# Kernel tuning notes

Hardware: AMD Instinct MI355X
Metric: run time of the kernel (lower is better)

Reference implementation:

```python
import jax, jax.numpy as jnp
import numpy as np
from jax import lax

DIM = 96
KS = 7
EPS = 1e-6


def setup_inputs() -> dict:
    key = jax.random.key(0)
    ks = jax.random.split(key, 12)
    N, C, H, W = 64, DIM, 56, 56
    s = 0.02
    x = jax.random.normal(ks[0], (N, C, H, W), dtype=jnp.float32)
    dw_w = jax.random.normal(ks[1], (C, 1, KS, KS), dtype=jnp.float32) * s  # depthwise, OIHW with I=1
    dw_b = jnp.zeros((C,), dtype=jnp.float32)
    ln_g = jnp.ones((C,), dtype=jnp.float32)
    ln_b = jnp.zeros((C,), dtype=jnp.float32)
    w1 = jax.random.normal(ks[2], (4 * C, C), dtype=jnp.float32) * s   # torch Linear weight [out,in]
    b1 = jnp.zeros((4 * C,), dtype=jnp.float32)
    grn_g = jnp.zeros((4 * C,), dtype=jnp.float32)  # GRN gamma/beta init to 0 as in ConvNeXtV2
    grn_b = jnp.zeros((4 * C,), dtype=jnp.float32)
    w2 = jax.random.normal(ks[3], (C, 4 * C), dtype=jnp.float32) * s
    b2 = jnp.zeros((C,), dtype=jnp.float32)
    return {"x": x, "dw_w": dw_w, "dw_b": dw_b, "ln_g": ln_g, "ln_b": ln_b,
            "w1": w1, "b1": b1, "grn_g": grn_g, "grn_b": grn_b, "w2": w2, "b2": b2}


def reference(x, dw_w, dw_b, ln_g, ln_b, w1, b1, grn_g, grn_b, w2, b2):
    C = x.shape[1]
    pad = KS // 2
    # 7x7 depthwise conv, NCHW
    y = lax.conv_general_dilated(x, dw_w, window_strides=(1, 1),
                                 padding=[(pad, pad), (pad, pad)],
                                 dimension_numbers=("NCHW", "OIHW", "NCHW"),
                                 feature_group_count=C)
    y = y + dw_b[None, :, None, None]
    y = jnp.transpose(y, (0, 2, 3, 1))  # [N,H,W,C]
    # channels-last LayerNorm, eps=1e-6
    mu = jnp.mean(y, axis=-1, keepdims=True)
    var = jnp.mean(jnp.square(y - mu), axis=-1, keepdims=True)
    y = (y - mu) * lax.rsqrt(var + EPS) * ln_g + ln_b
    # pwconv1 -> GELU (exact erf, torch default)
    y = jnp.einsum("nhwc,fc->nhwf", y, w1) + b1
    y = jax.nn.gelu(y, approximate=False)
    # GRN over spatial dims
    gx = jnp.sqrt(jnp.sum(jnp.square(y), axis=(1, 2), keepdims=True))  # [N,1,1,4C]
    nx = gx / (jnp.mean(gx, axis=-1, keepdims=True) + EPS)
    y = grn_g * (y * nx) + grn_b + y
    # pwconv2
    y = jnp.einsum("nhwf,cf->nhwc", y, w2) + b2
    y = jnp.transpose(y, (0, 3, 1, 2))  # back to NCHW
    # drop_path=0.0 -> identity; residual add
    return x + y
```

## Files before the change

kernel.cpp:

```cpp
#include <hip/hip_runtime.h>
#include <hip/hip_bf16.h>
#include <math.h>

#define HW   3136
#define NIMG 64
#define M_TOT (NIMG * HW)

typedef __attribute__((ext_vector_type(8))) short bf16x8_t;
typedef __attribute__((ext_vector_type(4))) float f32x4_t;
typedef __bf16 bf16x2v __attribute__((ext_vector_type(2)));

__device__ __forceinline__ unsigned short f2bf(float f) {
  union { float f; unsigned u; } v; v.f = f;
  unsigned r = v.u + 0x7FFFu + ((v.u >> 16) & 1u);
  return (unsigned short)(r >> 16);
}
__device__ __forceinline__ float bf2f(unsigned short h) {
  union { unsigned u; float f; } v; v.u = ((unsigned)h) << 16;
  return v.f;
}

__device__ __forceinline__ float dot2bf(unsigned a, unsigned b, float c) {
#if __has_builtin(__builtin_amdgcn_fdot2_f32_bf16)
  return __builtin_amdgcn_fdot2_f32_bf16(__builtin_bit_cast(bf16x2v, a),
                                         __builtin_bit_cast(bf16x2v, b), c, false);
#else
  return c + bf2f((unsigned short)(a & 0xffffu)) * bf2f((unsigned short)(b & 0xffffu))
           + bf2f((unsigned short)(a >> 16)) * bf2f((unsigned short)(b >> 16));
#endif
}

__device__ __forceinline__ int xcd_swz(int bid0) {
  return ((bid0 & 7) * 392) + (bid0 >> 3);
}

__global__ void k0_swz(const float* __restrict__ wsrc, unsigned short* __restrict__ bsw,
                       int N, int K) {
  int idx = blockIdx.x * 256 + threadIdx.x;
  int total = (N / 16) * (K / 32) * 64;
  if (idx >= total) return;
  int l  = idx & 63;
  int fi = idx >> 6;
  int KT = K / 32;
  int nt = fi / KT, kt = fi - nt * KT;
  int nn = nt * 16 + (l & 15);
  int kb = kt * 32 + (l >> 4) * 8;
  const float* src = wsrc + (size_t)nn * K + kb;
  unsigned short* dst = bsw + (size_t)idx * 8;
#pragma unroll
  for (int j = 0; j < 8; j++) dst[j] = f2bf(src[j]);
}

__global__ void k0_b2p(const float* __restrict__ w2, const float* __restrict__ grnb,
                       const float* __restrict__ b2, float* __restrict__ b2p) {
  int c = blockIdx.x * blockDim.x + threadIdx.x;
  if (c >= 96) return;
  float s = b2[c];
  const float* wr = w2 + (size_t)c * 384;
  for (int f = 0; f < 384; f++) s += grnb[f] * wr[f];
  b2p[c] = s;
}

__global__ void k0w(const float* __restrict__ dww, unsigned short* __restrict__ wswz) {
  int i = blockIdx.x * 256 + threadIdx.x;
  if (i >= 96 * 56) return;
  int ch = i / 56, rem = i - ch * 56, dy = rem >> 3, dx = rem & 7;
  wswz[i] = (dx < 7) ? f2bf(dww[ch * 49 + dy * 7 + dx]) : (unsigned short)0;
}

__global__ __launch_bounds__(256, 3) void k12f(
    const float* __restrict__ x, const unsigned short* __restrict__ wswz,
    const float* __restrict__ dwb, const float* __restrict__ lng,
    const float* __restrict__ lnb, const unsigned short* __restrict__ B1,
    const float* __restrict__ b1, unsigned char* __restrict__ y1f8,
    float* __restrict__ gx2) {
  __shared__ char smem[28928];
  float* lnp = (float*)smem;
  unsigned short* xsh = (unsigned short*)(smem + 768);
  unsigned short (*ts)[104] = (unsigned short(*)[104])(smem + 15616);
  unsigned char* ytB = (unsigned char*)(smem + 768);

  const int t = threadIdx.x;
  const int bid = xcd_swz(blockIdx.x);
  const int n = bid / 49;
  const int tile = bid - n * 49;
  const int tr = tile / 7, tc = tile - tr * 7;
  const int h0 = tr * 8, w0 = tc * 8;

  if (t < 192) lnp[t] = (t < 96) ? lng[t] : lnb[t - 96];

  const int cch = t & 31, crow = t >> 5;
  const bool colInt = (tc >= 1) && (tc <= 5);
  const bool rowInt = (tr >= 1) && (tr <= 5);

  int g_r[7], g_ch[7], g_wb[7];
  bool g_hok[7];
#pragma unroll
  for (int k = 0; k < 7; k++) {
    int i = t + k * 256;
    int cq = i & 3;
    int rc = i >> 2;
    g_r[k] = rc % 14; g_ch[k] = rc / 14;
    g_wb[k] = w0 + cq * 4 - 3;
    g_hok[k] = (unsigned)(h0 + g_r[k] - 3) < 56u;
  }

  float4 raw[3][7];
#pragma unroll
  for (int cc = 0; cc < 3; cc++) {
#pragma unroll
    for (int k = 0; k < 7; k++) {
      const int h = h0 + g_r[k] - 3;
      const int wb = g_wb[k];
      const float* xb = x + (size_t)(n * 96 + cc * 32 + g_ch[k]) * HW + h * 56 + wb;
      float4 v;
      if (rowInt && colInt) {
        v = *(const float4*)xb;
      } else {
        v = make_float4(0.f, 0.f, 0.f, 0.f);
        if (g_hok[k]) {
          if (colInt) {
            v = *(const float4*)xb;
          } else {
            if ((unsigned)(wb + 0) < 56u) v.x = xb[0];
            if ((unsigned)(wb + 1) < 56u) v.y = xb[1];
            if ((unsigned)(wb + 2) < 56u) v.z = xb[2];
            if ((unsigned)(wb + 3) < 56u) v.w = xb[3];
          }
        }
      }
      raw[cc][k] = v;
    }
  }

#pragma unroll
  for (int cc = 0; cc < 3; cc++) {
    const int c0 = cc * 32;
    if (cc) __syncthreads();
#pragma unroll
    for (int k = 0; k < 7; k++) {
      float4 v = raw[cc][k];
      uint2 u;
      u.x = (unsigned)f2bf(v.x) | ((unsigned)f2bf(v.y) << 16);
      u.y = (unsigned)f2bf(v.z) | ((unsigned)f2bf(v.w) << 16);
      *(uint2*)&xsh[g_ch[k] * 232 + g_r[k] * 16 + (g_wb[k] - w0 + 3)] = u;
    }
    bf16x8_t wv[7];
#pragma unroll
    for (int dy = 0; dy < 7; dy++)
      wv[dy] = *(const bf16x8_t*)&wswz[(size_t)(c0 + cch) * 56 + dy * 8];
    const float bias = dwb[c0 + cch];
    __syncthreads();
    float acc[8];
#pragma unroll
    for (int j = 0; j < 8; j++) acc[j] = bias;
#pragma unroll
    for (int dy = 0; dy < 7; dy++) {
      const unsigned* pr = (const unsigned*)&xsh[cch * 232 + (crow + dy) * 16];
      uint4 pa = *(const uint4*)pr;
      uint4 pb = *(const uint4*)(pr + 4);
      unsigned p[8] = {pa.x, pa.y, pa.z, pa.w, pb.x, pb.y, pb.z, pb.w};
      unsigned q[7];
#pragma unroll
      for (int i = 0; i < 7; i++) q[i] = (p[i] >> 16) | (p[i + 1] << 16);
      const unsigned* wu = (const unsigned*)&wv[dy];
#pragma unroll
      for (int j = 0; j < 8; j += 2) {
        int b = j >> 1;
        acc[j] = dot2bf(wu[3], p[b + 3],
                 dot2bf(wu[2], p[b + 2],
                 dot2bf(wu[1], p[b + 1],
                 dot2bf(wu[0], p[b + 0], acc[j]))));
        acc[j + 1] = dot2bf(wu[3], q[b + 3],
                     dot2bf(wu[2], q[b + 2],
                     dot2bf(wu[1], q[b + 1],
                     dot2bf(wu[0], q[b + 0], acc[j + 1]))));
      }
    }
#pragma unroll
    for (int j = 0; j < 8; j++)
      ts[crow * 8 + j][c0 + cch] = f2bf(acc[j]);
  }
  __syncthreads();

  {
    const int px = t >> 2, q = t & 3;
    const unsigned onebf = 0x3F803F80u;
    unsigned vu[12];
    float s = 0.f, ss = 0.f;
#pragma unroll
    for (int j = 0; j < 12; j++) {
      vu[j] = *(const unsigned*)&ts[px][q * 24 + j * 2];
      s  = dot2bf(vu[j], onebf, s);
      ss = dot2bf(vu[j], vu[j], ss);
    }
    s  += __shfl_xor(s, 1);  s  += __shfl_xor(s, 2);
    ss += __shfl_xor(ss, 1); ss += __shfl_xor(ss, 2);
    float mu  = s * (1.f / 96.f);
    float var = ss * (1.f / 96.f) - mu * mu;
    float rs  = rsqrtf(var + 1e-6f);
#pragma unroll
    for (int j = 0; j < 12; j++) {
      int ch = q * 24 + j * 2;
      float v0 = bf2f((unsigned short)(vu[j] & 0xffffu));
      float v1 = bf2f((unsigned short)(vu[j] >> 16));
      float o0 = (v0 - mu) * rs * lnp[ch] + lnp[96 + ch];
      float o1 = (v1 - mu) * rs * lnp[ch + 1] + lnp[96 + ch + 1];
      *(unsigned*)&ts[px][ch] = (unsigned)f2bf(o0) | ((unsigned)f2bf(o1) << 16);
    }
  }
  __syncthreads();
  const int wv_ = t >> 6, l = t & 63;
  const int lg = l >> 4, lr = l & 15;
  bf16x8_t af[4][3];
#pragma unroll
  for (int mt = 0; mt < 4; mt++)
#pragma unroll
    for (int kt = 0; kt < 3; kt++)
      af[mt][kt] = *(const bf16x8_t*)&ts[mt * 16 + lr][kt * 32 + lg * 8];
  __syncthreads();

  for (int half = 0; half < 2; half++) {
    for (int i = 0; i < 3; i++) {
      const int ntl = wv_ * 3 + i;
      const int nt  = half * 12 + ntl;
      bf16x8_t bf[3];
#pragma unroll
      for (int kt = 0; kt < 3; kt++)
        bf[kt] = *(const bf16x8_t*)(B1 + ((size_t)(nt * 3 + kt) * 64 + l) * 8);
      f32x4_t acc[4];
#pragma unroll
      for (int mt = 0; mt < 4; mt++) {
        f32x4_t a = {0.f, 0.f, 0.f, 0.f};
#pragma unroll
        for (int kt = 0; kt < 3; kt++)
          a = __builtin_amdgcn_mfma_f32_16x16x32_bf16(af[mt][kt], bf[kt], a, 0, 0, 0);
        acc[mt] = a;
      }
      const int f0 = nt * 16, fl0 = ntl * 16;
      float bias = b1[f0 + lr];
      float s2 = 0.f;
#pragma unroll
      for (int mt = 0; mt < 4; mt++) {
#pragma unroll
        for (int r = 0; r < 4; r++) {
          float v = acc[mt][r] + bias;
          float sq = v * v;
          float pe = fmaf(sq, -0.10295294f, -2.3021183f);
          float e  = __builtin_amdgcn_exp2f(v * pe);
          float g  = v * __builtin_amdgcn_rcpf(1.f + e);
          s2 += g * g;
          unsigned p8 = (unsigned)__builtin_amdgcn_cvt_pk_fp8_f32(g, g, 0, false);
          ytB[(mt * 16 + lg * 4 + r) * 200 + fl0 + lr] = (unsigned char)p8;
        }
      }
      s2 += __shfl_xor(s2, 16);
      s2 += __shfl_xor(s2, 32);
      if (l < 16) atomicAdd(gx2 + n * 384 + f0 + l, s2);
    }
    __syncthreads();
#pragma unroll
    for (int it = 0; it < 6; it++) {
      int id = t + it * 256;
      int mt = id / 384, ktl = (id >> 6) % 6, ll = id & 63;
      unsigned long long d =
        *(const unsigned long long*)&ytB[(mt * 16 + (ll & 15)) * 200 + ktl * 32 + (ll >> 4) * 8];
      *(unsigned long long*)(y1f8 +
        (((size_t)(bid * 4 + mt) * 12 + half * 6 + ktl) * 64 + ll) * 8) = d;
    }
    __syncthreads();
  }
}

__global__ __launch_bounds__(256) void k3_coefB(
    const float* __restrict__ gx2, const float* __restrict__ grng,
    const unsigned short* __restrict__ B2, unsigned char* __restrict__ B2s8) {
  __shared__ float red[256];
  __shared__ float cf[384];
  const int n = blockIdx.x, t = threadIdx.x;
  float s = 0.f;
  for (int f = t; f < 384; f += 256) {
    float g = sqrtf(gx2[n * 384 + f]);
    cf[f] = g; s += g;
  }
  red[t] = s; __syncthreads();
  for (int o = 128; o > 0; o >>= 1) {
    if (t < o) red[t] += red[t + o];
    __syncthreads();
  }
  float inv = 1.f / (red[0] * (1.f / 384.f) + 1e-6f);
  for (int f = t; f < 384; f += 256)
    cf[f] = 1.f + grng[f] * cf[f] * inv;
  __syncthreads();
  unsigned char* dstn = B2s8 + (size_t)n * 36864;
  for (int i = t; i < 4608; i += 256) {
    int e0 = i * 8;
    int fi = e0 >> 9, ll = (e0 & 511) >> 3;
    int kb = (fi % 12) * 32 + (ll >> 4) * 8;
    uint4 w = *(const uint4*)(B2 + e0);
    const unsigned* wu = (const unsigned*)&w;
    float vv[8];
#pragma unroll
    for (int h = 0; h < 4; h++) {
      vv[h * 2 + 0] = bf2f((unsigned short)(wu[h] & 0xffffu)) * cf[kb + h * 2];
      vv[h * 2 + 1] = bf2f((unsigned short)(wu[h] >> 16)) * cf[kb + h * 2 + 1];
    }
    unsigned p0 = (unsigned)__builtin_amdgcn_cvt_pk_fp8_f32(vv[0], vv[1], 0, false);
    p0 = (unsigned)__builtin_amdgcn_cvt_pk_fp8_f32(vv[2], vv[3], p0, true);
    unsigned p1 = (unsigned)__builtin_amdgcn_cvt_pk_fp8_f32(vv[4], vv[5], 0, false);
    p1 = (unsigned)__builtin_amdgcn_cvt_pk_fp8_f32(vv[6], vv[7], p1, true);
    uint2 o; o.x = p0; o.y = p1;
    *(uint2*)(dstn + e0) = o;
  }
}

__global__ __launch_bounds__(256) void k4_gemm2(
    const unsigned char* __restrict__ y1f8, const unsigned char* __restrict__ B2s8,
    const float* __restrict__ b2p, const float* __restrict__ x,
    float* __restrict__ out) {
  __shared__ float zt[96][68];
  const int t  = threadIdx.x;
  const int wv = t >> 6, l = t & 63;
  const int lg = l >> 4, lr = l & 15;
  const int bid = xcd_swz(blockIdx.x);
  const int n = bid / 49;
  const int tile = bid - n * 49;
  const int tr = tile / 7, tc = tile - tr * 7;
  const unsigned char* Bn = B2s8 + (size_t)n * 36864;

  long af[12];
  const unsigned char* ap = y1f8 + ((size_t)(bid * 4 + wv) * 12) * 512 + l * 8;
#pragma unroll
  for (int kt = 0; kt < 12; kt++)
    af[kt] = *(const long*)(ap + kt * 512);

  f32x4_t acc[6];
#pragma unroll
  for (int i = 0; i < 6; i++) acc[i] = (f32x4_t){0.f, 0.f, 0.f, 0.f};
#pragma unroll
  for (int kt = 0; kt < 12; kt++) {
#pragma unroll
    for (int nt = 0; nt < 6; nt++) {
      long b = *(const long*)(Bn + ((size_t)(nt * 12 + kt) * 64 + l) * 8);
      acc[nt] = __builtin_amdgcn_mfma_f32_16x16x32_fp8_fp8(af[kt], b, acc[nt], 0, 0, 0);
    }
  }
#pragma unroll
  for (int nt = 0; nt < 6; nt++) {
    int c = nt * 16 + lr;
#pragma unroll
    for (int r = 0; r < 4; r++)
      zt[c][wv * 16 + lg * 4 + r] = acc[nt][r];
  }
  __syncthreads();
#pragma unroll
  for (int it = 0; it < 6; it++) {
    int id = t + it * 256;
    int c = id >> 4, q = id & 15;
    int row = q >> 1, jq = (q & 1) * 4;
    float4 z = *(const float4*)&zt[c][row * 8 + jq];
    size_t base = ((size_t)(n * 96 + c)) * HW + (size_t)(tr * 8 + row) * 56 + tc * 8 + jq;
    float4 xv = *(const float4*)(x + base);
    float bp = b2p[c];
    float4 o;
    o.x = xv.x + z.x + bp;
    o.y = xv.y + z.y + bp;
    o.z = xv.z + z.z + bp;
    o.w = xv.w + z.w + bp;
    *(float4*)(out + base) = o;
  }
}

extern "C" void kernel_launch(void* const* d_in, const int* in_sizes, int n_in,
                              void* d_out, int out_size, void* d_ws, size_t ws_size,
                              hipStream_t stream) {
  const float* x    = (const float*)d_in[0];
  const float* dww  = (const float*)d_in[1];
  const float* dwb  = (const float*)d_in[2];
  const float* lng  = (const float*)d_in[3];
  const float* lnb  = (const float*)d_in[4];
  const float* w1   = (const float*)d_in[5];
  const float* b1   = (const float*)d_in[6];
  const float* grng = (const float*)d_in[7];
  const float* grnb = (const float*)d_in[8];
  const float* w2   = (const float*)d_in[9];
  const float* b2   = (const float*)d_in[10];
  float* out = (float*)d_out;

  char* ws = (char*)d_ws;
  size_t off = 0;
  auto alloc = [&](size_t bytes) {
    char* p = ws + off;
    off += (bytes + 255) & ~(size_t)255;
    return p;
  };
  unsigned char*  y1f8 = (unsigned char*)alloc((size_t)M_TOT * 384);
  unsigned char*  B2s8 = (unsigned char*)alloc((size_t)64 * 36864);
  unsigned short* B1sw = (unsigned short*)alloc((size_t)384 * 96 * 2);
  unsigned short* B2sw = (unsigned short*)alloc((size_t)96 * 384 * 2);
  unsigned short* wswz = (unsigned short*)alloc((size_t)96 * 56 * 2);
  float* gx2  = (float*)alloc((size_t)64 * 384 * 4);
  float* b2p  = (float*)alloc((size_t)96 * 4);
  if (off > ws_size) return;

  hipMemsetAsync(gx2, 0, 64 * 384 * 4, stream);
  k0_swz<<<18, 256, 0, stream>>>(w1, B1sw, 384, 96);
  k0_swz<<<18, 256, 0, stream>>>(w2, B2sw, 96, 384);
  k0_b2p<<<1, 128, 0, stream>>>(w2, grnb, b2, b2p);
  k0w<<<21, 256, 0, stream>>>(dww, wswz);
  k12f<<<3136, 256, 0, stream>>>(x, wswz, dwb, lng, lnb, B1sw, b1, y1f8, gx2);
  k3_coefB<<<64, 256, 0, stream>>>(gx2, grng, B2sw, B2s8);
  k4_gemm2<<<3136, 256, 0, stream>>>(y1f8, B2s8, b2p, x, out);
}
```

Before: 183.2 us.

## Compute GEMM1 transposed so GELU output writes fp8 fragments directly, drop LDS staging

The first pointwise GEMM now uses the weights as the A operand and the normalized activations as B. Each lane's accumulator then holds four consecutive hidden features, which pack straight into the fp8 layout GEMM2 expects and go to global memory without staging through shared memory, removing two barriers per half. GRN sum-of-squares partials stay in registers until the end and are reduced by shuffle, so fewer atomics are issued. The w2 swizzle kernel is dropped and the coefficient kernel reads fp32 w2 directly, at the cost of more register pressure in the fused kernel.

```diff
diff --git a/kernel.cpp b/kernel.cpp
--- a/kernel.cpp
+++ b/kernel.cpp
@@ -78,7 +78,6 @@
   float* lnp = (float*)smem;
   unsigned short* xsh = (unsigned short*)(smem + 768);
   unsigned short (*ts)[104] = (unsigned short(*)[104])(smem + 15616);
-  unsigned char* ytB = (unsigned char*)(smem + 768);
 
   const int t = threadIdx.x;
   const int bid = xcd_swz(blockIdx.x);
@@ -210,71 +209,88 @@
     }
   }
   __syncthreads();
+
   const int wv_ = t >> 6, l = t & 63;
   const int lg = l >> 4, lr = l & 15;
-  bf16x8_t af[4][3];
-#pragma unroll
-  for (int mt = 0; mt < 4; mt++)
-#pragma unroll
-    for (int kt = 0; kt < 3; kt++)
-      af[mt][kt] = *(const bf16x8_t*)&ts[mt * 16 + lr][kt * 32 + lg * 8];
-  __syncthreads();
-
-  for (int half = 0; half < 2; half++) {
-    for (int i = 0; i < 3; i++) {
-      const int ntl = wv_ * 3 + i;
-      const int nt  = half * 12 + ntl;
-      bf16x8_t bf[3];
-#pragma unroll
-      for (int kt = 0; kt < 3; kt++)
-        bf[kt] = *(const bf16x8_t*)(B1 + ((size_t)(nt * 3 + kt) * 64 + l) * 8);
-      f32x4_t acc[4];
-#pragma unroll
-      for (int mt = 0; mt < 4; mt++) {
-        f32x4_t a = {0.f, 0.f, 0.f, 0.f};
-#pragma unroll
-        for (int kt = 0; kt < 3; kt++)
-          a = __builtin_amdgcn_mfma_f32_16x16x32_bf16(af[mt][kt], bf[kt], a, 0, 0, 0);
-        acc[mt] = a;
+  bf16x8_t bfr[4][3];
+#pragma unroll
+  for (int nt = 0; nt < 4; nt++)
+#pragma unroll
+    for (int kc = 0; kc < 3; kc++)
+      bfr[nt][kc] = *(const bf16x8_t*)&ts[nt * 16 + lr][kc * 32 + lg * 8];
+
+  float s2a[6][4];
+#pragma unroll
+  for (int i = 0; i < 6; i++)
+#pragma unroll
+    for (int r = 0; r < 4; r++) s2a[i][r] = 0.f;
+  unsigned qprev[4];
+
+#pragma unroll
+  for (int ftl = 0; ftl < 6; ftl++) {
+    const int ft = wv_ * 6 + ftl;
+    bf16x8_t aw[3];
+#pragma unroll
+    for (int kc = 0; kc < 3; kc++)
+      aw[kc] = *(const bf16x8_t*)(B1 + ((size_t)(ft * 3 + kc) * 64 + l) * 8);
+    float4 bq = *(const float4*)(b1 + ft * 16 + lg * 4);
+    f32x4_t acc[4];
+#pragma unroll
+    for (int nt = 0; nt < 4; nt++) acc[nt] = (f32x4_t){0.f, 0.f, 0.f, 0.f};
+#pragma unroll
+    for (int kc = 0; kc < 3; kc++)
+#pragma unroll
+      for (int nt = 0; nt < 4; nt++)
+        acc[nt] = __builtin_amdgcn_mfma_f32_16x16x32_bf16(aw[kc], bfr[nt][kc], acc[nt], 0, 0, 0);
+    unsigned qcur[4];
+#pragma unroll
+    for (int nt = 0; nt < 4; nt++) {
+      float g[4];
+#pragma unroll
+      for (int r = 0; r < 4; r++) {
+        float v = acc[nt][r] + ((const float*)&bq)[r];
+        float sq = v * v;
+        float pe = fmaf(sq, -0.10295294f, -2.3021183f);
+        float e  = __builtin_amdgcn_exp2f(v * pe);
+        float gg = v * __builtin_amdgcn_rcpf(1.f + e);
+        g[r] = gg;
+        s2a[ftl][r] += gg * gg;
       }
-      const int f0 = nt * 16, fl0 = ntl * 16;
-      float bias = b1[f0 + lr];
-      float s2 = 0.f;
-#pragma unroll
-      for (int mt = 0; mt < 4; mt++) {
-#pragma unroll
-        for (int r = 0; r < 4; r++) {
-          float v = acc[mt][r] + bias;
-          float sq = v * v;
-          float pe = fmaf(sq, -0.10295294f, -2.3021183f);
-          float e  = __builtin_amdgcn_exp2f(v * pe);
-          float g  = v * __builtin_amdgcn_rcpf(1.f + e);
-          s2 += g * g;
-          unsigned p8 = (unsigned)__builtin_amdgcn_cvt_pk_fp8_f32(g, g, 0, false);
-          ytB[(mt * 16 + lg * 4 + r) * 200 + fl0 + lr] = (unsigned char)p8;
-        }
+      unsigned p = (unsigned)__builtin_amdgcn_cvt_pk_fp8_f32(g[0], g[1], 0, false);
+      p = (unsigned)__builtin_amdgcn_cvt_pk_fp8_f32(g[2], g[3], p, true);
+      qcur[nt] = p;
+    }
+    if (ftl & 1) {
+      const int ktl = ftl >> 1;
+#pragma unroll
+      for (int nt = 0; nt < 4; nt++) {
+        unsigned long long d = (unsigned long long)qprev[nt] |
+                               ((unsigned long long)qcur[nt] << 32);
+        *(unsigned long long*)(y1f8 +
+          (((size_t)(bid * 4 + nt) * 12 + wv_ * 3 + ktl) * 64 + l) * 8) = d;
       }
-      s2 += __shfl_xor(s2, 16);
-      s2 += __shfl_xor(s2, 32);
-      if (l < 16) atomicAdd(gx2 + n * 384 + f0 + l, s2);
-    }
-    __syncthreads();
-#pragma unroll
-    for (int it = 0; it < 6; it++) {
-      int id = t + it * 256;
-      int mt = id / 384, ktl = (id >> 6) % 6, ll = id & 63;
-      unsigned long long d =
-        *(const unsigned long long*)&ytB[(mt * 16 + (ll & 15)) * 200 + ktl * 32 + (ll >> 4) * 8];
-      *(unsigned long long*)(y1f8 +
-        (((size_t)(bid * 4 + mt) * 12 + half * 6 + ktl) * 64 + ll) * 8) = d;
-    }
-    __syncthreads();
+    } else {
+#pragma unroll
+      for (int nt = 0; nt < 4; nt++) qprev[nt] = qcur[nt];
+    }
+  }
+
+#pragma unroll
+  for (int ftl = 0; ftl < 6; ftl++) {
+#pragma unroll
+    for (int r = 0; r < 4; r++) {
+      float v = s2a[ftl][r];
+      v += __shfl_xor(v, 1); v += __shfl_xor(v, 2);
+      v += __shfl_xor(v, 4); v += __shfl_xor(v, 8);
+      if (lr == 0)
+        atomicAdd(gx2 + n * 384 + (wv_ * 6 + ftl) * 16 + lg * 4 + r, v);
+    }
   }
 }
 
 __global__ __launch_bounds__(256) void k3_coefB(
     const float* __restrict__ gx2, const float* __restrict__ grng,
-    const unsigned short* __restrict__ B2, unsigned char* __restrict__ B2s8) {
+    const float* __restrict__ w2, unsigned char* __restrict__ B2s8) {
   __shared__ float red[256];
   __shared__ float cf[384];
   const int n = blockIdx.x, t = threadIdx.x;
@@ -294,23 +310,25 @@
   __syncthreads();
   unsigned char* dstn = B2s8 + (size_t)n * 36864;
   for (int i = t; i < 4608; i += 256) {
-    int e0 = i * 8;
-    int fi = e0 >> 9, ll = (e0 & 511) >> 3;
-    int kb = (fi % 12) * 32 + (ll >> 4) * 8;
-    uint4 w = *(const uint4*)(B2 + e0);
-    const unsigned* wu = (const unsigned*)&w;
+    int fi = i >> 6, ll = i & 63;
+    int kt = fi % 12, nt = fi / 12;
+    int lg = ll >> 4, lr = ll & 15;
+    int c  = nt * 16 + lr;
+    int f0 = kt * 32 + lg * 4;
+    const float* wr = w2 + (size_t)c * 384;
+    float4 wa = *(const float4*)(wr + f0);
+    float4 wb = *(const float4*)(wr + f0 + 16);
     float vv[8];
-#pragma unroll
-    for (int h = 0; h < 4; h++) {
-      vv[h * 2 + 0] = bf2f((unsigned short)(wu[h] & 0xffffu)) * cf[kb + h * 2];
-      vv[h * 2 + 1] = bf2f((unsigned short)(wu[h] >> 16)) * cf[kb + h * 2 + 1];
-    }
+    vv[0] = wa.x * cf[f0 + 0];  vv[1] = wa.y * cf[f0 + 1];
+    vv[2] = wa.z * cf[f0 + 2];  vv[3] = wa.w * cf[f0 + 3];
+    vv[4] = wb.x * cf[f0 + 16]; vv[5] = wb.y * cf[f0 + 17];
+    vv[6] = wb.z * cf[f0 + 18]; vv[7] = wb.w * cf[f0 + 19];
     unsigned p0 = (unsigned)__builtin_amdgcn_cvt_pk_fp8_f32(vv[0], vv[1], 0, false);
     p0 = (unsigned)__builtin_amdgcn_cvt_pk_fp8_f32(vv[2], vv[3], p0, true);
     unsigned p1 = (unsigned)__builtin_amdgcn_cvt_pk_fp8_f32(vv[4], vv[5], 0, false);
     p1 = (unsigned)__builtin_amdgcn_cvt_pk_fp8_f32(vv[6], vv[7], p1, true);
     uint2 o; o.x = p0; o.y = p1;
-    *(uint2*)(dstn + e0) = o;
+    *(uint2*)(dstn + (size_t)i * 8) = o;
   }
 }
 
@@ -397,7 +415,6 @@
   unsigned char*  y1f8 = (unsigned char*)alloc((size_t)M_TOT * 384);
   unsigned char*  B2s8 = (unsigned char*)alloc((size_t)64 * 36864);
   unsigned short* B1sw = (unsigned short*)alloc((size_t)384 * 96 * 2);
-  unsigned short* B2sw = (unsigned short*)alloc((size_t)96 * 384 * 2);
   unsigned short* wswz = (unsigned short*)alloc((size_t)96 * 56 * 2);
   float* gx2  = (float*)alloc((size_t)64 * 384 * 4);
   float* b2p  = (float*)alloc((size_t)96 * 4);
@@ -405,10 +422,9 @@
 
   hipMemsetAsync(gx2, 0, 64 * 384 * 4, stream);
   k0_swz<<<18, 256, 0, stream>>>(w1, B1sw, 384, 96);
-  k0_swz<<<18, 256, 0, stream>>>(w2, B2sw, 96, 384);
   k0_b2p<<<1, 128, 0, stream>>>(w2, grnb, b2, b2p);
   k0w<<<21, 256, 0, stream>>>(dww, wswz);
   k12f<<<3136, 256, 0, stream>>>(x, wswz, dwb, lng, lnb, B1sw, b1, y1f8, gx2);
-  k3_coefB<<<64, 256, 0, stream>>>(gx2, grng, B2sw, B2s8);
+  k3_coefB<<<64, 256, 0, stream>>>(gx2, grng, w2, B2s8);
   k4_gemm2<<<3136, 256, 0, stream>>>(y1f8, B2s8, b2p, x, out);
 }
```

New measurement: 196.7 us. 7.4% more time.

## Use 512-thread blocks in fused dwconv/LN/GEMM1 kernel, splitting per-thread work

Applied to the files above, without the earlier changes.

Doubles the threads per block of the fused depthwise-conv, LayerNorm and first-GEMM kernel from 256 to 512. Each thread now computes 4 output columns instead of 8 in the depthwise conv. Each thread covers 12 channels instead of 24 in the LayerNorm. Each of 8 waves computes 3 feature tiles over the full 384 outputs in one pass, which removes the two-half loop and its extra barriers. The aim is more parallelism and latency hiding per tile, plus fewer barriers. In exchange, the launch bound of 4 blocks of 512 threads tightens the register budget and risks spills, and the staging buffer in shared memory grows.

```diff
diff --git a/kernel.cpp b/kernel.cpp
--- a/kernel.cpp
+++ b/kernel.cpp
@@ -68,7 +68,7 @@
   wswz[i] = (dx < 7) ? f2bf(dww[ch * 49 + dy * 7 + dx]) : (unsigned short)0;
 }
 
-__global__ __launch_bounds__(256, 3) void k12f(
+__global__ __launch_bounds__(512, 4) void k12f(
     const float* __restrict__ x, const unsigned short* __restrict__ wswz,
     const float* __restrict__ dwb, const float* __restrict__ lng,
     const float* __restrict__ lnb, const unsigned short* __restrict__ B1,
@@ -89,15 +89,20 @@
 
   if (t < 192) lnp[t] = (t < 96) ? lng[t] : lnb[t - 96];
 
-  const int cch = t & 31, crow = t >> 5;
+  const int cch = t & 31;
+  const int row = (t >> 5) & 7;
+  const int hc  = t >> 8;
+  const int cb  = hc * 4;
   const bool colInt = (tc >= 1) && (tc <= 5);
   const bool rowInt = (tr >= 1) && (tr <= 5);
 
-  int g_r[7], g_ch[7], g_wb[7];
-  bool g_hok[7];
-#pragma unroll
-  for (int k = 0; k < 7; k++) {
-    int i = t + k * 256;
+  int g_r[4], g_ch[4], g_wb[4];
+  bool g_hok[4], g_ok[4];
+#pragma unroll
+  for (int k = 0; k < 4; k++) {
+    int slot = t + k * 512;
+    g_ok[k] = slot < 1792;
+    int i = g_ok[k] ? slot : 0;
     int cq = i & 3;
     int rc = i >> 2;
     g_r[k] = rc % 14; g_ch[k] = rc / 14;
@@ -105,20 +110,19 @@
     g_hok[k] = (unsigned)(h0 + g_r[k] - 3) < 56u;
   }
 
-  float4 raw[3][7];
+  float4 raw[3][4];
 #pragma unroll
   for (int cc = 0; cc < 3; cc++) {
 #pragma unroll
-    for (int k = 0; k < 7; k++) {
-      const int h = h0 + g_r[k] - 3;
-      const int wb = g_wb[k];
-      const float* xb = x + (size_t)(n * 96 + cc * 32 + g_ch[k]) * HW + h * 56 + wb;
-      float4 v;
-      if (rowInt && colInt) {
-        v = *(const float4*)xb;
-      } else {
-        v = make_float4(0.f, 0.f, 0.f, 0.f);
-        if (g_hok[k]) {
+    for (int k = 0; k < 4; k++) {
+      float4 v = make_float4(0.f, 0.f, 0.f, 0.f);
+      if (g_ok[k]) {
+        const int h = h0 + g_r[k] - 3;
+        const int wb = g_wb[k];
+        const float* xb = x + (size_t)(n * 96 + cc * 32 + g_ch[k]) * HW + h * 56 + wb;
+        if (rowInt && colInt) {
+          v = *(const float4*)xb;
+        } else if (g_hok[k]) {
           if (colInt) {
             v = *(const float4*)xb;
           } else {
@@ -138,12 +142,14 @@
     const int c0 = cc * 32;
     if (cc) __syncthreads();
 #pragma unroll
-    for (int k = 0; k < 7; k++) {
-      float4 v = raw[cc][k];
-      uint2 u;
-      u.x = (unsigned)f2bf(v.x) | ((unsigned)f2bf(v.y) << 16);
-      u.y = (unsigned)f2bf(v.z) | ((unsigned)f2bf(v.w) << 16);
-      *(uint2*)&xsh[g_ch[k] * 232 + g_r[k] * 16 + (g_wb[k] - w0 + 3)] = u;
+    for (int k = 0; k < 4; k++) {
+      if (g_ok[k]) {
+        float4 v = raw[cc][k];
+        uint2 u;
+        u.x = (unsigned)f2bf(v.x) | ((unsigned)f2bf(v.y) << 16);
+        u.y = (unsigned)f2bf(v.z) | ((unsigned)f2bf(v.w) << 16);
+        *(uint2*)&xsh[g_ch[k] * 232 + g_r[k] * 16 + (g_wb[k] - w0 + 3)] = u;
+      }
     }
     bf16x8_t wv[7];
 #pragma unroll
@@ -151,57 +157,56 @@
       wv[dy] = *(const bf16x8_t*)&wswz[(size_t)(c0 + cch) * 56 + dy * 8];
     const float bias = dwb[c0 + cch];
     __syncthreads();
-    float acc[8];
-#pragma unroll
-    for (int j = 0; j < 8; j++) acc[j] = bias;
+    float acc[4];
+#pragma unroll
+    for (int j = 0; j < 4; j++) acc[j] = bias;
 #pragma unroll
     for (int dy = 0; dy < 7; dy++) {
-      const unsigned* pr = (const unsigned*)&xsh[cch * 232 + (crow + dy) * 16];
+      const unsigned* pr = (const unsigned*)&xsh[cch * 232 + (row + dy) * 16];
       uint4 pa = *(const uint4*)pr;
       uint4 pb = *(const uint4*)(pr + 4);
-      unsigned p[8] = {pa.x, pa.y, pa.z, pa.w, pb.x, pb.y, pb.z, pb.w};
-      unsigned q[7];
-#pragma unroll
-      for (int i = 0; i < 7; i++) q[i] = (p[i] >> 16) | (p[i + 1] << 16);
+      unsigned s8[8] = {pa.x, pa.y, pa.z, pa.w, pb.x, pb.y, pb.z, pb.w};
+      unsigned P[6];
+#pragma unroll
+      for (int i = 0; i < 6; i++) P[i] = hc ? s8[i + 2] : s8[i];
+      unsigned Q[5];
+#pragma unroll
+      for (int i = 0; i < 5; i++) Q[i] = (P[i] >> 16) | (P[i + 1] << 16);
       const unsigned* wu = (const unsigned*)&wv[dy];
-#pragma unroll
-      for (int j = 0; j < 8; j += 2) {
-        int b = j >> 1;
-        acc[j] = dot2bf(wu[3], p[b + 3],
-                 dot2bf(wu[2], p[b + 2],
-                 dot2bf(wu[1], p[b + 1],
-                 dot2bf(wu[0], p[b + 0], acc[j]))));
-        acc[j + 1] = dot2bf(wu[3], q[b + 3],
-                     dot2bf(wu[2], q[b + 2],
-                     dot2bf(wu[1], q[b + 1],
-                     dot2bf(wu[0], q[b + 0], acc[j + 1]))));
-      }
-    }
-#pragma unroll
-    for (int j = 0; j < 8; j++)
-      ts[crow * 8 + j][c0 + cch] = f2bf(acc[j]);
+      acc[0] = dot2bf(wu[3], P[3], dot2bf(wu[2], P[2],
+               dot2bf(wu[1], P[1], dot2bf(wu[0], P[0], acc[0]))));
+      acc[1] = dot2bf(wu[3], Q[3], dot2bf(wu[2], Q[2],
+               dot2bf(wu[1], Q[1], dot2bf(wu[0], Q[0], acc[1]))));
+      acc[2] = dot2bf(wu[3], P[4], dot2bf(wu[2], P[3],
+               dot2bf(wu[1], P[2], dot2bf(wu[0], P[1], acc[2]))));
+      acc[3] = dot2bf(wu[3], Q[4], dot2bf(wu[2], Q[3],
+               dot2bf(wu[1], Q[2], dot2bf(wu[0], Q[1], acc[3]))));
+    }
+#pragma unroll
+    for (int j = 0; j < 4; j++)
+      ts[row * 8 + cb + j][c0 + cch] = f2bf(acc[j]);
   }
   __syncthreads();
 
   {
-    const int px = t >> 2, q = t & 3;
+    const int px = t >> 3, q = t & 7;
     const unsigned onebf = 0x3F803F80u;
-    unsigned vu[12];
+    unsigned vu[6];
     float s = 0.f, ss = 0.f;
 #pragma unroll
-    for (int j = 0; j < 12; j++) {
-      vu[j] = *(const unsigned*)&ts[px][q * 24 + j * 2];
+    for (int j = 0; j < 6; j++) {
+      vu[j] = *(const unsigned*)&ts[px][q * 12 + j * 2];
       s  = dot2bf(vu[j], onebf, s);
       ss = dot2bf(vu[j], vu[j], ss);
     }
-    s  += __shfl_xor(s, 1);  s  += __shfl_xor(s, 2);
-    ss += __shfl_xor(ss, 1); ss += __shfl_xor(ss, 2);
+    s  += __shfl_xor(s, 1);  s  += __shfl_xor(s, 2);  s  += __shfl_xor(s, 4);
+    ss += __shfl_xor(ss, 1); ss += __shfl_xor(ss, 2); ss += __shfl_xor(ss, 4);
     float mu  = s * (1.f / 96.f);
     float var = ss * (1.f / 96.f) - mu * mu;
     float rs  = rsqrtf(var + 1e-6f);
 #pragma unroll
-    for (int j = 0; j < 12; j++) {
-      int ch = q * 24 + j * 2;
+    for (int j = 0; j < 6; j++) {
+      int ch = q * 12 + j * 2;
       float v0 = bf2f((unsigned short)(vu[j] & 0xffffu));
       float v1 = bf2f((unsigned short)(vu[j] >> 16));
       float o0 = (v0 - mu) * rs * lnp[ch] + lnp[96 + ch];
@@ -220,55 +225,53 @@
       af[mt][kt] = *(const bf16x8_t*)&ts[mt * 16 + lr][kt * 32 + lg * 8];
   __syncthreads();
 
-  for (int half = 0; half < 2; half++) {
-    for (int i = 0; i < 3; i++) {
-      const int ntl = wv_ * 3 + i;
-      const int nt  = half * 12 + ntl;
-      bf16x8_t bf[3];
+#pragma unroll
+  for (int ftl = 0; ftl < 3; ftl++) {
+    const int ft = wv_ * 3 + ftl;
+    bf16x8_t bf[3];
+#pragma unroll
+    for (int kt = 0; kt < 3; kt++)
+      bf[kt] = *(const bf16x8_t*)(B1 + ((size_t)(ft * 3 + kt) * 64 + l) * 8);
+    f32x4_t acc[4];
+#pragma unroll
+    for (int mt = 0; mt < 4; mt++) {
+      f32x4_t a = {0.f, 0.f, 0.f, 0.f};
 #pragma unroll
       for (int kt = 0; kt < 3; kt++)
-        bf[kt] = *(const bf16x8_t*)(B1 + ((size_t)(nt * 3 + kt) * 64 + l) * 8);
-      f32x4_t acc[4];
-#pragma unroll
-      for (int mt = 0; mt < 4; mt++) {
-        f32x4_t a = {0.f, 0.f, 0.f, 0.f};
-#pragma unroll
-        for (int kt = 0; kt < 3; kt++)
-          a = __builtin_amdgcn_mfma_f32_16x16x32_bf16(af[mt][kt], bf[kt], a, 0, 0, 0);
-        acc[mt] = a;
+        a = __builtin_amdgcn_mfma_f32_16x16x32_bf16(af[mt][kt], bf[kt], a, 0, 0, 0);
+      acc[mt] = a;
+    }
+    const int f0 = ft * 16;
+    float bias = b1[f0 + lr];
+    float s2 = 0.f;
+#pragma unroll
+    for (int mt = 0; mt < 4; mt++) {
+#pragma unroll
+      for (int r = 0; r < 4; r++) {
+        float v = acc[mt][r] + bias;
+        float sq = v * v;
+        float pe = fmaf(sq, -0.10295294f, -2.3021183f);
+        float e  = __builtin_amdgcn_exp2f(v * pe);
+        float g  = v * __builtin_amdgcn_rcpf(1.f + e);
+        s2 += g * g;
+        unsigned p8 = (unsigned)__builtin_amdgcn_cvt_pk_fp8_f32(g, g, 0, false);
+        ytB[(mt * 16 + lg * 4 + r) * 400 + f0 + lr] = (unsigned char)p8;
       }
-      const int f0 = nt * 16, fl0 = ntl * 16;
-      float bias = b1[f0 + lr];
-      float s2 = 0.f;
-#pragma unroll
-      for (int mt = 0; mt < 4; mt++) {
-#pragma unroll
-        for (int r = 0; r < 4; r++) {
-          float v = acc[mt][r] + bias;
-          float sq = v * v;
-          float pe = fmaf(sq, -0.10295294f, -2.3021183f);
-          float e  = __builtin_amdgcn_exp2f(v * pe);
-          float g  = v * __builtin_amdgcn_rcpf(1.f + e);
-          s2 += g * g;
-          unsigned p8 = (unsigned)__builtin_amdgcn_cvt_pk_fp8_f32(g, g, 0, false);
-          ytB[(mt * 16 + lg * 4 + r) * 200 + fl0 + lr] = (unsigned char)p8;
-        }
-      }
-      s2 += __shfl_xor(s2, 16);
-      s2 += __shfl_xor(s2, 32);
-      if (l < 16) atomicAdd(gx2 + n * 384 + f0 + l, s2);
-    }
-    __syncthreads();
-#pragma unroll
-    for (int it = 0; it < 6; it++) {
-      int id = t + it * 256;
-      int mt = id / 384, ktl = (id >> 6) % 6, ll = id & 63;
-      unsigned long long d =
-        *(const unsigned long long*)&ytB[(mt * 16 + (ll & 15)) * 200 + ktl * 32 + (ll >> 4) * 8];
-      *(unsigned long long*)(y1f8 +
-        (((size_t)(bid * 4 + mt) * 12 + half * 6 + ktl) * 64 + ll) * 8) = d;
-    }
-    __syncthreads();
+    }
+    s2 += __shfl_xor(s2, 16);
+    s2 += __shfl_xor(s2, 32);
+    if (l < 16) atomicAdd(gx2 + n * 384 + f0 + l, s2);
+  }
+  __syncthreads();
+#pragma unroll
+  for (int k = 0; k < 6; k++) {
+    int id = t + k * 512;
+    int mt = id / 768, rest = id - mt * 768;
+    int kt = rest >> 6, ll = rest & 63;
+    unsigned long long d =
+      *(const unsigned long long*)&ytB[(mt * 16 + (ll & 15)) * 400 + kt * 32 + (ll >> 4) * 8];
+    *(unsigned long long*)(y1f8 +
+      (((size_t)(bid * 4 + mt) * 12 + kt) * 64 + ll) * 8) = d;
   }
 }
 
@@ -408,7 +411,7 @@
   k0_swz<<<18, 256, 0, stream>>>(w2, B2sw, 96, 384);
   k0_b2p<<<1, 128, 0, stream>>>(w2, grnb, b2, b2p);
   k0w<<<21, 256, 0, stream>>>(dww, wswz);
-  k12f<<<3136, 256, 0, stream>>>(x, wswz, dwb, lng, lnb, B1sw, b1, y1f8, gx2);
+  k12f<<<3136, 512, 0, stream>>>(x, wswz, dwb, lng, lnb, B1sw, b1, y1f8, gx2);
   k3_coefB<<<64, 256, 0, stream>>>(gx2, grng, B2sw, B2s8);
   k4_gemm2<<<3136, 256, 0, stream>>>(y1f8, B2s8, b2p, x, out);
 }
```

After: 205.1 us. 11.9% more time.
